# Optimization experiments

Hardware: AMD Instinct MI355X
Metric: run time of the kernel (lower is better)

The kernel has to match this reference:

```python
import jax, jax.numpy as jnp
import numpy as np

VOCAB, D, H, L, SEQ = 32000, 768, 12, 6, 1024
HD = D // H
DFF = 4 * D
EPS = 1e-5


def _ln(x, g, b):
    mu = jnp.mean(x, axis=-1, keepdims=True)
    var = jnp.var(x, axis=-1, keepdims=True)
    return (x - mu) * jax.lax.rsqrt(var + EPS) * g + b


def setup_inputs() -> dict:
    key = jax.random.key(0)
    ks = jax.random.split(key, 10)
    s = lambda *sh: 0.02
    return {
        "idx": jax.random.randint(ks[0], (2, SEQ), 0, VOCAB, dtype=jnp.int64) if jax.config.jax_enable_x64 else jax.random.randint(ks[0], (2, SEQ), 0, VOCAB, dtype=jnp.int32),
        "tok_emb": jax.random.normal(ks[1], (VOCAB, D), jnp.float32) * 0.02,
        "pos_emb": jax.random.normal(ks[2], (SEQ, D), jnp.float32) * 0.02,
        "Wqkv": jax.random.normal(ks[3], (L, D, 3 * D), jnp.float32) * 0.02,
        "bqkv": jnp.zeros((L, 3 * D), jnp.float32),
        "Wo": jax.random.normal(ks[4], (L, D, D), jnp.float32) * 0.02,
        "bo": jnp.zeros((L, D), jnp.float32),
        "ln1_g": jnp.ones((L, D), jnp.float32),
        "ln1_b": jnp.zeros((L, D), jnp.float32),
        "ln2_g": jnp.ones((L, D), jnp.float32),
        "ln2_b": jnp.zeros((L, D), jnp.float32),
        "W1": jax.random.normal(ks[5], (L, D, DFF), jnp.float32) * 0.02,
        "b1": jnp.zeros((L, DFF), jnp.float32),
        "W2": jax.random.normal(ks[6], (L, DFF, D), jnp.float32) * 0.02,
        "b2": jnp.zeros((L, D), jnp.float32),
        "lnf_g": jnp.ones((D,), jnp.float32),
        "lnf_b": jnp.zeros((D,), jnp.float32),
        "Wlm": jax.random.normal(ks[7], (D, VOCAB), jnp.float32) * 0.02,
    }


def _forward(idx, tok_emb, pos_emb, Wqkv, bqkv, Wo, bo, ln1_g, ln1_b,
             ln2_g, ln2_b, W1, b1, W2, b2, lnf_g, lnf_b, Wlm):
    B, T = idx.shape
    x = tok_emb[idx] + pos_emb[None, :T]  # [B,T,D]
    causal = jnp.tril(jnp.ones((T, T), bool))  # [T,T]
    for l in range(L):
        h = _ln(x, ln1_g[l], ln1_b[l])
        qkv = h @ Wqkv[l] + bqkv[l]  # [B,T,3D]
        qkv = qkv.reshape(B, T, 3, H, HD).transpose(2, 0, 3, 1, 4)
        q, k, v = qkv[0], qkv[1], qkv[2]  # each [B,H,T,HD]
        att = jnp.einsum('bhqd,bhkd->bhqk', q, k) / np.sqrt(HD).astype(np.float32)
        att = jnp.where(causal, att, -jnp.inf)
        att = jax.nn.softmax(att, axis=-1)
        o = jnp.einsum('bhqk,bhkd->bhqd', att, v)
        o = o.transpose(0, 2, 1, 3).reshape(B, T, D)
        x = x + o @ Wo[l] + bo[l]
        h = _ln(x, ln2_g[l], ln2_b[l])
        x = x + jax.nn.gelu(h @ W1[l] + b1[l], approximate=False) @ W2[l] + b2[l]
    x = _ln(x, lnf_g, lnf_b)
    return x @ Wlm  # [B,T,VOCAB]


def reference(idx, tok_emb, pos_emb, Wqkv, bqkv, Wo, bo, ln1_g, ln1_b,
              ln2_g, ln2_b, W1, b1, W2, b2, lnf_g, lnf_b, Wlm):
    return _forward(idx, tok_emb, pos_emb, Wqkv, bqkv, Wo, bo, ln1_g, ln1_b,
                    ln2_g, ln2_b, W1, b1, W2, b2, lnf_g, lnf_b, Wlm)
```

## Files before the change

kernel.cpp:

```cpp
#include <hip/hip_runtime.h>
#include <math.h>

#define TT   1024
#define DD   768
#define HH   12
#define LLAY 6
#define DFFN 3072
#define BB   2
#define NTOK (BB*TT)

typedef __bf16 bf16;
typedef __attribute__((ext_vector_type(8))) __bf16 bf16x8;
typedef __attribute__((ext_vector_type(4))) __bf16 bf16x4;
typedef __attribute__((ext_vector_type(4))) float f32x4;

__device__ inline unsigned pack_bf16x2(float a, float b) {
    union { bf16 h[2]; unsigned u; } un;
    un.h[0] = (bf16)a; un.h[1] = (bf16)b;
    return un.u;
}

__device__ inline void gload16(const bf16* g, bf16* l) {
    __builtin_amdgcn_global_load_lds((const void*)g, (void*)l, 16, 0, 0);
}

template<int N> __device__ inline void waitcnt_vm() {
    if constexpr (N == 0) asm volatile("s_waitcnt vmcnt(0)" ::: "memory");
    else if constexpr (N == 3) asm volatile("s_waitcnt vmcnt(3)" ::: "memory");
    else if constexpr (N == 4) asm volatile("s_waitcnt vmcnt(4)" ::: "memory");
}

__global__ __launch_bounds__(256) void embed_kernel(const int* __restrict__ idx,
                                                    const float* __restrict__ tok,
                                                    const float* __restrict__ pos,
                                                    float* __restrict__ x) {
    int bt = blockIdx.x;
    int t  = bt % TT;
    int id = idx[bt];
    const float* te = tok + (size_t)id * DD;
    const float* pe = pos + (size_t)t * DD;
    float* xr = x + (size_t)bt * DD;
    for (int d = threadIdx.x; d < DD; d += 256) xr[d] = te[d] + pe[d];
}

__global__ __launch_bounds__(256) void ln_kernel(const float* __restrict__ in,
                                                 const float* __restrict__ g,
                                                 const float* __restrict__ b,
                                                 bf16* __restrict__ out) {
    const int wid = threadIdx.x >> 6, lane = threadIdx.x & 63;
    const int row = blockIdx.x * 4 + wid;
    const float* xr = in + (size_t)row * DD;
    float4 v[3];
    float s = 0.f, s2 = 0.f;
#pragma unroll
    for (int j = 0; j < 3; ++j) {
        v[j] = *(const float4*)&xr[lane * 4 + 256 * j];
        s  += v[j].x + v[j].y + v[j].z + v[j].w;
        s2 += v[j].x * v[j].x + v[j].y * v[j].y + v[j].z * v[j].z + v[j].w * v[j].w;
    }
    for (int off = 32; off; off >>= 1) { s += __shfl_down(s, off); s2 += __shfl_down(s2, off); }
    s = __shfl(s, 0); s2 = __shfl(s2, 0);
    const float mu = s / (float)DD;
    const float rs = rsqrtf(s2 / (float)DD - mu * mu + 1e-5f);
    bf16* orow = out + (size_t)row * DD;
#pragma unroll
    for (int j = 0; j < 3; ++j) {
        float4 gg = *(const float4*)&g[lane * 4 + 256 * j];
        float4 bb = *(const float4*)&b[lane * 4 + 256 * j];
        bf16x4 o;
        o[0] = (bf16)((v[j].x - mu) * rs * gg.x + bb.x);
        o[1] = (bf16)((v[j].y - mu) * rs * gg.y + bb.y);
        o[2] = (bf16)((v[j].z - mu) * rs * gg.z + bb.z);
        o[3] = (bf16)((v[j].w - mu) * rs * gg.w + bb.w);
        *(bf16x4*)&orow[lane * 4 + 256 * j] = o;
    }
}

__device__ inline void convT_tile64(const float* __restrict__ in, bf16* __restrict__ out,
                                    int K, int N, int k0, int n0) {
    __shared__ float tile[64][65];
    const int c = threadIdx.x & 63, q = threadIdx.x >> 6;
#pragma unroll
    for (int i = 0; i < 16; ++i)
        tile[q + i * 4][c] = in[(size_t)(k0 + q + i * 4) * N + n0 + c];
    __syncthreads();
#pragma unroll
    for (int i = 0; i < 16; ++i)
        out[(size_t)(n0 + q + i * 4) * K + k0 + c] = (bf16)tile[c][q + i * 4];
}

__global__ __launch_bounds__(256) void convT_kernel(const float* __restrict__ in,
                                                    bf16* __restrict__ out,
                                                    int K, int N) {
    convT_tile64(in, out, K, N, blockIdx.y * 64, blockIdx.x * 64);
}

__global__ __launch_bounds__(256) void convT4_kernel(const float* __restrict__ w0,
                                                     const float* __restrict__ w1,
                                                     const float* __restrict__ w2,
                                                     const float* __restrict__ w3,
                                                     bf16* __restrict__ o0,
                                                     bf16* __restrict__ o1,
                                                     bf16* __restrict__ o2,
                                                     bf16* __restrict__ o3) {
    int bid = blockIdx.x;
    const float* in; bf16* out; int K, N, t;
    if (bid < 432)       { in = w0; out = o0; K = 768;  N = 2304; t = bid; }
    else if (bid < 576)  { in = w1; out = o1; K = 768;  N = 768;  t = bid - 432; }
    else if (bid < 1152) { in = w2; out = o2; K = 768;  N = 3072; t = bid - 576; }
    else                 { in = w3; out = o3; K = 3072; N = 768;  t = bid - 1152; }
    int nt = N / 64;
    convT_tile64(in, out, K, N, (t / nt) * 64, (t % nt) * 64);
}

template<int BM, int EPI>
__global__ __launch_bounds__(256) void mgemm(const bf16* __restrict__ A,
                                             const bf16* __restrict__ Bt,
                                             const float* __restrict__ bias,
                                             const float* __restrict__ res,
                                             void* __restrict__ Cout,
                                             bf16* __restrict__ vtout,
                                             int M, int N, int K) {
    constexpr int MF = BM / 32;
    constexpr int NF = 4;
    constexpr int AIT = BM / 64;
    constexpr int STG = AIT + 2;
    constexpr int ASZ = BM * 32;
    constexpr int BUFE = ASZ + 128 * 32;
    __shared__ __align__(16) bf16 smem[3 * BUFE];
    int bm = blockIdx.y * BM;
    int bn = blockIdx.x * 128;
    int tid = threadIdx.x;
    int lane = tid & 63;
    int w = tid >> 6;
    int wr = w >> 1, wc = w & 1;
    int l15 = lane & 15, g = lane >> 4;

    f32x4 acc[MF][NF];
#pragma unroll
    for (int m = 0; m < MF; ++m)
#pragma unroll
        for (int n = 0; n < NF; ++n) acc[m][n] = (f32x4){0.f, 0.f, 0.f, 0.f};

    int r = lane >> 2;
    int koff = ((lane & 3) ^ ((r >> 1) & 3)) * 8;
    const bf16* Ab = A + (size_t)(bm + w * 16 + r) * K + koff;
    const bf16* Bb = Bt + (size_t)(bn + w * 16 + r) * K + koff;

    auto stage = [&](int p, int k0) {
        bf16* base = smem + p * BUFE;
        bf16* Asb = base + w * 16 * 32;
        bf16* Bsb = base + ASZ + w * 16 * 32;
#pragma unroll
        for (int it = 0; it < AIT; ++it)
            gload16(Ab + (size_t)(it * 64) * K + k0, Asb + it * 64 * 32);
#pragma unroll
        for (int it = 0; it < 2; ++it)
            gload16(Bb + (size_t)(it * 64) * K + k0, Bsb + it * 64 * 32);
    };

    stage(0, 0);
    stage(1, 32);
    waitcnt_vm<STG>();
    __builtin_amdgcn_s_barrier();
    int cur = 0;

    for (int k0 = 0; k0 < K; k0 += 32) {
        const bf16* Ac = smem + cur * BUFE;
        const bf16* Bc = Ac + ASZ;
        bf16x8 af[MF], bfv[NF];
#pragma unroll
        for (int m = 0; m < MF; ++m) {
            int row = wr * (BM / 2) + m * 16 + l15;
            int gs = g ^ ((row >> 1) & 3);
            af[m] = *(const bf16x8*)&Ac[row * 32 + gs * 8];
        }
#pragma unroll
        for (int n = 0; n < NF; ++n) {
            int row = wc * 64 + n * 16 + l15;
            int gs = g ^ ((row >> 1) & 3);
            bfv[n] = *(const bf16x8*)&Bc[row * 32 + gs * 8];
        }
        bool st = (k0 + 64 < K);
        if (st) {
            int nxt = cur + 2; if (nxt >= 3) nxt -= 3;
            stage(nxt, k0 + 64);
        }
#pragma unroll
        for (int m = 0; m < MF; ++m)
#pragma unroll
            for (int n = 0; n < NF; ++n)
                acc[m][n] = __builtin_amdgcn_mfma_f32_16x16x32_bf16(af[m], bfv[n], acc[m][n], 0, 0, 0);
        if (st) waitcnt_vm<STG>();
        else    waitcnt_vm<0>();
        __builtin_amdgcn_s_barrier();
        cur = (cur == 2) ? 0 : cur + 1;
    }

    int lq = g * 4;
#pragma unroll
    for (int m = 0; m < MF; ++m) {
#pragma unroll
        for (int n = 0; n < NF; ++n) {
            int col = bn + wc * 64 + n * 16 + l15;
            float bv = bias[col];
            if (EPI == 4 && col >= 2 * DD) {
                int row0 = bm + wr * (BM / 2) + m * 16 + lq;
                int b = row0 >> 10, t0 = row0 & 1023;
                int hd = col - 2 * DD;
                union { bf16 h[4]; unsigned long long u; } pk;
#pragma unroll
                for (int j = 0; j < 4; ++j) pk.h[j] = (bf16)(acc[m][n][j] + bv);
                *(unsigned long long*)&vtout[((size_t)(b * DD + hd)) * TT + t0] = pk.u;
            } else {
#pragma unroll
                for (int j = 0; j < 4; ++j) {
                    int row = bm + wr * (BM / 2) + m * 16 + lq + j;
                    float v = acc[m][n][j] + bv;
                    if (EPI == 2) {
                        ((float*)Cout)[(size_t)row * N + col] = v + res[(size_t)row * N + col];
                    } else if (EPI == 3) {
                        v = 0.5f * v * (1.f + erff(v * 0.70710678118654752f));
                        ((bf16*)Cout)[(size_t)row * N + col] = (bf16)v;
                    } else if (EPI == 1) {
                        ((bf16*)Cout)[(size_t)row * N + col] = (bf16)v;
                    } else {
                        if (col < DD) v *= 0.125f;
                        ((bf16*)Cout)[(size_t)row * N + col] = (bf16)v;
                    }
                }
            }
        }
    }
}

__global__ __launch_bounds__(512, 2) void lmgemm(const bf16* __restrict__ A,
                                                 const bf16* __restrict__ Bt,
                                                 float* __restrict__ C) {
    constexpr int BUFE = 2 * 256 * 64;
    __shared__ __align__(16) bf16 smem[2 * BUFE];
    const int orig = blockIdx.x;
    const int xcd = orig & 7, local = orig >> 3;
    const int bnb = xcd * 16 + (local >> 3);
    if (bnb >= 125) return;
    const int bm = (local & 7) * 256;
    const int bn = bnb * 256;
    const int tid = threadIdx.x;
    const int w = tid >> 6, lane = tid & 63;
    const int wm = w >> 2, wn = w & 3;
    const int l15 = lane & 15, g = lane >> 4;

    const int swzr = (l15 >> 1) & 7;
    const int pc0 = (g ^ swzr) * 8;

    const int r8 = lane >> 3, c8 = lane & 7;
    const bf16* agp[4]; const bf16* bgp[4];
    int aldso[4], bldso[4];
#pragma unroll
    for (int j = 0; j < 4; ++j) {
        int br = w * 32 + j * 8 + r8;
        int swz = (br >> 1) & 7;
        agp[j] = A  + (size_t)(bm + br) * DD + (c8 ^ swz) * 8;
        bgp[j] = Bt + (size_t)(bn + br) * DD + (c8 ^ swz) * 8;
        aldso[j] = (w * 32 + j * 8) * 64;
        bldso[j] = 256 * 64 + (w * 32 + j * 8) * 64;
    }

    f32x4 acc[8][4];
#pragma unroll
    for (int m = 0; m < 8; ++m)
#pragma unroll
        for (int n = 0; n < 4; ++n) acc[m][n] = (f32x4){0.f, 0.f, 0.f, 0.f};

    {
        bf16* base = smem;
#pragma unroll
        for (int j = 0; j < 4; ++j) gload16(agp[j], base + aldso[j]);
#pragma unroll
        for (int j = 0; j < 4; ++j) gload16(bgp[j], base + bldso[j]);
    }
    __syncthreads();
    int cur = 0;

    for (int t = 0; t < 12; ++t) {
        const bf16* Ar = smem + cur * BUFE;
        const bf16* Br = Ar + 256 * 64;
        bf16* nbase = smem + (cur ^ 1) * BUFE;
        const int k0n = (t + 1) * 64;
        const bool st = (t < 11);
        if (st) {
#pragma unroll
            for (int j = 0; j < 4; ++j) gload16(agp[j] + k0n, nbase + aldso[j]);
        }
        bf16x8 af[8], bfv[4];
#pragma unroll
        for (int m = 0; m < 8; ++m)
            af[m] = *(const bf16x8*)&Ar[(wm * 128 + m * 16 + l15) * 64 + pc0];
#pragma unroll
        for (int n = 0; n < 4; ++n)
            bfv[n] = *(const bf16x8*)&Br[(wn * 64 + n * 16 + l15) * 64 + pc0];
        __builtin_amdgcn_s_setprio(1);
#pragma unroll
        for (int m = 0; m < 8; ++m)
#pragma unroll
            for (int n = 0; n < 4; ++n)
                acc[m][n] = __builtin_amdgcn_mfma_f32_16x16x32_bf16(af[m], bfv[n], acc[m][n], 0, 0, 0);
        __builtin_amdgcn_s_setprio(0);
        if (st) {
#pragma unroll
            for (int j = 0; j < 4; ++j) gload16(bgp[j] + k0n, nbase + bldso[j]);
        }
#pragma unroll
        for (int m = 0; m < 8; ++m)
            af[m] = *(const bf16x8*)&Ar[(wm * 128 + m * 16 + l15) * 64 + (pc0 ^ 32)];
#pragma unroll
        for (int n = 0; n < 4; ++n)
            bfv[n] = *(const bf16x8*)&Br[(wn * 64 + n * 16 + l15) * 64 + (pc0 ^ 32)];
        __builtin_amdgcn_s_setprio(1);
#pragma unroll
        for (int m = 0; m < 8; ++m)
#pragma unroll
            for (int n = 0; n < 4; ++n)
                acc[m][n] = __builtin_amdgcn_mfma_f32_16x16x32_bf16(af[m], bfv[n], acc[m][n], 0, 0, 0);
        __builtin_amdgcn_s_setprio(0);
        __syncthreads();
        cur ^= 1;
    }

    float* eb = (float*)smem + w * (16 * 68);
    const int rr = lane >> 2, c0 = (lane & 3) * 16;
#pragma unroll
    for (int mf = 0; mf < 8; ++mf) {
#pragma unroll
        for (int n = 0; n < 4; ++n)
#pragma unroll
            for (int j = 0; j < 4; ++j)
                eb[(g * 4 + j) * 68 + n * 16 + l15] = acc[mf][n][j];
        asm volatile("s_waitcnt lgkmcnt(0)" ::: "memory");
        const float* src = &eb[rr * 68 + c0];
        float* dst = C + (size_t)(bm + wm * 128 + mf * 16 + rr) * 32000 + bn + wn * 64 + c0;
        *(float4*)(dst + 0)  = *(const float4*)(src + 0);
        *(float4*)(dst + 4)  = *(const float4*)(src + 4);
        *(float4*)(dst + 8)  = *(const float4*)(src + 8);
        *(float4*)(dst + 12) = *(const float4*)(src + 12);
    }
}

__global__ __launch_bounds__(256) void fattn_kernel(const bf16* __restrict__ qkv,
                                                    const bf16* __restrict__ vt,
                                                    bf16* __restrict__ o) {
    const int bh = blockIdx.y;
    const int b = bh / HH, h = bh % HH;
    const int qc = gridDim.x - 1 - blockIdx.x;
    const int q0 = qc * 64;
    const int tid = threadIdx.x;
    const int w = tid >> 6, lane = tid & 63;
    const int l15 = lane & 15, g = lane >> 4;

    __shared__ __align__(16) bf16 Ks[64 * 64];
    __shared__ __align__(16) bf16 Vs[64 * 64];
    __shared__ __align__(16) bf16 Ps[4][16 * 64];

    const size_t basebt = (size_t)b * TT;
    const int qw = q0 + w * 16;
    const int qg = qw + l15;

    bf16x8 bq0, bq1;
    {
        const bf16* qp = qkv + (basebt + qw + l15) * 2304 + h * 64 + g * 8;
        bq0 = *(const bf16x8*)(qp);
        bq1 = *(const bf16x8*)(qp + 32);
    }

    float mstate = -1e30f, lstate = 0.f;
    f32x4 oacc[4];
#pragma unroll
    for (int nf = 0; nf < 4; ++nf) oacc[nf] = (f32x4){0.f, 0.f, 0.f, 0.f};

    const int swzA = (l15 & 7) << 4;
    char* const psBase = (char*)&Ps[w][0];

    const int r0 = tid >> 3;
    const int e0 = (tid & 7) * 8;
    bf16x8 kreg[2], vreg[2];
#pragma unroll
    for (int i = 0; i < 2; ++i) {
        int r = r0 + 32 * i;
        kreg[i] = *(const bf16x8*)&qkv[(basebt + r) * 2304 + DD + h * 64 + e0];
        vreg[i] = *(const bf16x8*)&vt[((size_t)bh * 64 + r) * TT + e0];
    }

    const int nchunk = qc + 1;
    for (int c = 0; c < nchunk; ++c) {
        const int kc = c * 64;
#pragma unroll
        for (int i = 0; i < 2; ++i) {
            int r = r0 + 32 * i;
            int swzW = (r & 7) << 4;
            *(bf16x8*)((char*)Ks + r * 128 + ((e0 * 2) ^ swzW)) = kreg[i];
            *(bf16x8*)((char*)Vs + r * 128 + ((e0 * 2) ^ swzW)) = vreg[i];
        }
        __syncthreads();
        if (c + 1 < nchunk) {
            const int kc2 = kc + 64;
#pragma unroll
            for (int i = 0; i < 2; ++i) {
                int r = r0 + 32 * i;
                kreg[i] = *(const bf16x8*)&qkv[(basebt + kc2 + r) * 2304 + DD + h * 64 + e0];
                vreg[i] = *(const bf16x8*)&vt[((size_t)bh * 64 + r) * TT + kc2 + e0];
            }
        }
        if (kc <= qw + 15) {
            f32x4 s[4];
            __builtin_amdgcn_s_setprio(1);
#pragma unroll
            for (int mf = 0; mf < 4; ++mf) {
                char* kr = (char*)Ks + (16 * mf + l15) * 128;
                bf16x8 ka0 = *(const bf16x8*)(kr + ((16 * g) ^ swzA));
                bf16x8 ka1 = *(const bf16x8*)(kr + ((64 + 16 * g) ^ swzA));
                f32x4 a = (f32x4){0.f, 0.f, 0.f, 0.f};
                a = __builtin_amdgcn_mfma_f32_16x16x32_bf16(ka0, bq0, a, 0, 0, 0);
                a = __builtin_amdgcn_mfma_f32_16x16x32_bf16(ka1, bq1, a, 0, 0, 0);
                s[mf] = a;
            }
            __builtin_amdgcn_s_setprio(0);
            if (kc + 63 > qw) {
#pragma unroll
                for (int mf = 0; mf < 4; ++mf)
#pragma unroll
                    for (int j = 0; j < 4; ++j)
                        if (kc + 16 * mf + 4 * g + j > qg) s[mf][j] = -1e30f;
            }
            float cm = -1e30f;
#pragma unroll
            for (int mf = 0; mf < 4; ++mf)
#pragma unroll
                for (int j = 0; j < 4; ++j) cm = fmaxf(cm, s[mf][j]);
            cm = fmaxf(cm, __shfl_xor(cm, 16));
            cm = fmaxf(cm, __shfl_xor(cm, 32));
            float mnew = fmaxf(mstate, cm);
            float sc = __expf(mstate - mnew);
            mstate = mnew;
            float p[4][4];
            float psum = 0.f;
#pragma unroll
            for (int mf = 0; mf < 4; ++mf)
#pragma unroll
                for (int j = 0; j < 4; ++j) { float pv = __expf(s[mf][j] - mnew); p[mf][j] = pv; psum += pv; }
            psum += __shfl_xor(psum, 16);
            psum += __shfl_xor(psum, 32);
            lstate = lstate * sc + psum;
#pragma unroll
            for (int mf = 0; mf < 4; ++mf) {
                unsigned lo = pack_bf16x2(p[mf][0], p[mf][1]);
                unsigned hi = pack_bf16x2(p[mf][2], p[mf][3]);
                char* dst = psBase + l15 * 128 + ((32 * mf + 8 * g) ^ swzA);
                *(unsigned*)dst = lo;
                *(unsigned*)(dst + 4) = hi;
            }
            float s0 = __shfl(sc, 4 * g + 0), s1 = __shfl(sc, 4 * g + 1);
            float s2 = __shfl(sc, 4 * g + 2), s3 = __shfl(sc, 4 * g + 3);
#pragma unroll
            for (int nf = 0; nf < 4; ++nf) {
                oacc[nf][0] *= s0; oacc[nf][1] *= s1; oacc[nf][2] *= s2; oacc[nf][3] *= s3;
            }
            bf16x8 pa0 = *(const bf16x8*)(psBase + l15 * 128 + ((16 * g) ^ swzA));
            bf16x8 pa1 = *(const bf16x8*)(psBase + l15 * 128 + ((64 + 16 * g) ^ swzA));
            __builtin_amdgcn_s_setprio(1);
#pragma unroll
            for (int nf = 0; nf < 4; ++nf) {
                char* vr = (char*)Vs + (16 * nf + l15) * 128;
                bf16x8 vb0 = *(const bf16x8*)(vr + ((16 * g) ^ swzA));
                bf16x8 vb1 = *(const bf16x8*)(vr + ((64 + 16 * g) ^ swzA));
                oacc[nf] = __builtin_amdgcn_mfma_f32_16x16x32_bf16(pa0, vb0, oacc[nf], 0, 0, 0);
                oacc[nf] = __builtin_amdgcn_mfma_f32_16x16x32_bf16(pa1, vb1, oacc[nf], 0, 0, 0);
            }
            __builtin_amdgcn_s_setprio(0);
        }
        __syncthreads();
    }
    float linv = 1.f / lstate;
    float l0 = __shfl(linv, 4 * g + 0), l1 = __shfl(linv, 4 * g + 1);
    float l2 = __shfl(linv, 4 * g + 2), l3 = __shfl(linv, 4 * g + 3);
    float lj[4] = {l0, l1, l2, l3};
#pragma unroll
    for (int j = 0; j < 4; ++j) {
        bf16* orow = o + (size_t)(basebt + qw + 4 * g + j) * DD + h * 64 + l15;
#pragma unroll
        for (int nf = 0; nf < 4; ++nf)
            orow[16 * nf] = (bf16)(oacc[nf][j] * lj[j]);
    }
}

extern "C" void kernel_launch(void* const* d_in, const int* in_sizes, int n_in,
                              void* d_out, int out_size, void* d_ws, size_t ws_size,
                              hipStream_t stream) {
    (void)in_sizes; (void)n_in; (void)out_size; (void)ws_size;
    const int*   idx  = (const int*)d_in[0];
    const float* tok  = (const float*)d_in[1];
    const float* pos  = (const float*)d_in[2];
    const float* Wqkv = (const float*)d_in[3];
    const float* bqkv = (const float*)d_in[4];
    const float* Wo   = (const float*)d_in[5];
    const float* bo   = (const float*)d_in[6];
    const float* ln1g = (const float*)d_in[7];
    const float* ln1b = (const float*)d_in[8];
    const float* ln2g = (const float*)d_in[9];
    const float* ln2b = (const float*)d_in[10];
    const float* W1   = (const float*)d_in[11];
    const float* b1   = (const float*)d_in[12];
    const float* W2   = (const float*)d_in[13];
    const float* b2   = (const float*)d_in[14];
    const float* lnfg = (const float*)d_in[15];
    const float* lnfb = (const float*)d_in[16];
    const float* Wlm  = (const float*)d_in[17];
    float* out = (float*)d_out;

    char* ws = (char*)d_ws;
    float* x     = (float*)(ws);
    bf16*  abuf0 = (bf16*)(ws + 6291456);
    bf16*  abuf1 = (bf16*)(ws + 9437184);
    bf16*  qkvb  = (bf16*)(ws + 22020096);
    bf16*  vtb   = (bf16*)(ws + 31457280);
    bf16*  wbuf  = (bf16*)(ws + 34603008);

    bf16* wq = wbuf;
    bf16* wo = wbuf + 1769472;
    bf16* w1 = wbuf + 2359296;
    bf16* w2 = wbuf + 4718592;

    embed_kernel<<<NTOK, 256, 0, stream>>>(idx, tok, pos, x);

    for (int l = 0; l < LLAY; ++l) {
        convT4_kernel<<<1728, 256, 0, stream>>>(
            Wqkv + (size_t)l * DD * 3 * DD, Wo + (size_t)l * DD * DD,
            W1 + (size_t)l * DD * DFFN, W2 + (size_t)l * DFFN * DD,
            wq, wo, w1, w2);
        ln_kernel<<<NTOK / 4, 256, 0, stream>>>(x, ln1g + l * DD, ln1b + l * DD, abuf0);
        mgemm<128, 4><<<dim3(3 * DD / 128, NTOK / 128), 256, 0, stream>>>(
            abuf0, wq, bqkv + (size_t)l * 3 * DD, nullptr, qkvb, vtb, NTOK, 3 * DD, DD);
        fattn_kernel<<<dim3(TT / 64, BB * HH), 256, 0, stream>>>(qkvb, vtb, abuf0);
        mgemm<64, 2><<<dim3(DD / 128, NTOK / 64), 256, 0, stream>>>(
            abuf0, wo, bo + (size_t)l * DD, x, x, nullptr, NTOK, DD, DD);
        ln_kernel<<<NTOK / 4, 256, 0, stream>>>(x, ln2g + l * DD, ln2b + l * DD, abuf0);
        mgemm<128, 3><<<dim3(DFFN / 128, NTOK / 128), 256, 0, stream>>>(
            abuf0, w1, b1 + (size_t)l * DFFN, nullptr, abuf1, nullptr, NTOK, DFFN, DD);
        mgemm<64, 2><<<dim3(DD / 128, NTOK / 64), 256, 0, stream>>>(
            abuf1, w2, b2 + (size_t)l * DD, x, x, nullptr, NTOK, DD, DFFN);
    }
    ln_kernel<<<NTOK / 4, 256, 0, stream>>>(x, lnfg, lnfb, abuf0);
    convT_kernel<<<dim3(32000 / 64, DD / 64), 256, 0, stream>>>(Wlm, wbuf, DD, 32000);
    lmgemm<<<1024, 512, 0, stream>>>(abuf0, wbuf, out);
}
```

Before: 982.5 us.

## Add 256x128 double-buffered bgemm for QKV/FFN1 and shrink lmgemm K-tile

Adds a new bgemm kernel with 512 threads, 256x128 block tiles, a 32-wide K step and two-stage LDS double buffering, and uses it for the QKV and FFN-up projections in place of the 128-tile mgemm. The lm-head GEMM is also switched from a 64-wide K tile split into two half-steps to a simpler 32-wide K tile with 24 iterations, which halves its LDS footprint. The intent is more per-block reuse and fewer, larger blocks for the projection GEMMs, plus a simpler schedule for the lm-head. The trade-offs are more barriers per unit of K and reduced prefetch depth compared with the three-stage mgemm pipeline.

```diff
diff --git a/kernel.cpp b/kernel.cpp
--- a/kernel.cpp
+++ b/kernel.cpp
@@ -204,8 +204,99 @@
         for (int n = 0; n < NF; ++n) {
             int col = bn + wc * 64 + n * 16 + l15;
             float bv = bias[col];
+#pragma unroll
+            for (int j = 0; j < 4; ++j) {
+                int row = bm + wr * (BM / 2) + m * 16 + lq + j;
+                float v = acc[m][n][j] + bv;
+                if (EPI == 2) {
+                    ((float*)Cout)[(size_t)row * N + col] = v + res[(size_t)row * N + col];
+                } else if (EPI == 3) {
+                    v = 0.5f * v * (1.f + erff(v * 0.70710678118654752f));
+                    ((bf16*)Cout)[(size_t)row * N + col] = (bf16)v;
+                } else {
+                    ((bf16*)Cout)[(size_t)row * N + col] = (bf16)v;
+                }
+            }
+        }
+    }
+    (void)vtout;
+}
+
+template<int EPI>
+__global__ __launch_bounds__(512, 2) void bgemm(const bf16* __restrict__ A,
+                                                const bf16* __restrict__ Bt,
+                                                const float* __restrict__ bias,
+                                                void* __restrict__ Cout,
+                                                bf16* __restrict__ vtout,
+                                                int N, int K) {
+    constexpr int ABUF = 256 * 32;
+    constexpr int BUFE = ABUF + 128 * 32;
+    __shared__ __align__(16) bf16 smem[2 * BUFE];
+    const int bm = blockIdx.y * 256;
+    const int bn = blockIdx.x * 128;
+    const int tid = threadIdx.x;
+    const int w = tid >> 6, lane = tid & 63;
+    const int wm = w >> 1, wn = w & 1;
+    const int l15 = lane & 15, g = lane >> 4;
+
+    const int fcol = (g ^ ((l15 >> 1) & 3)) * 8;
+
+    const int rA = lane >> 2;
+    const int csw = ((lane & 3) ^ ((lane >> 3) & 3)) * 8;
+    const bf16* a0 = A  + (size_t)(bm + w * 16 + rA) * K + csw;
+    const bf16* b0 = Bt + (size_t)(bn + w * 16 + rA) * K + csw;
+    const int ld0 = (w * 16) * 32;
+    const int ld1 = (w * 16 + 128) * 32;
+
+    f32x4 acc[4][4];
+#pragma unroll
+    for (int m = 0; m < 4; ++m)
+#pragma unroll
+        for (int n = 0; n < 4; ++n) acc[m][n] = (f32x4){0.f, 0.f, 0.f, 0.f};
+
+    auto stagef = [&](int p, int kelem) {
+        bf16* base = smem + p * BUFE;
+        gload16(a0 + kelem, base + ld0);
+        gload16(a0 + (size_t)128 * K + kelem, base + ld1);
+        gload16(b0 + kelem, base + ABUF + ld0);
+    };
+
+    stagef(0, 0);
+    __syncthreads();
+    int cur = 0;
+
+    const int NT = K / 32;
+    for (int t = 0; t < NT; ++t) {
+        if (t + 1 < NT) stagef(cur ^ 1, (t + 1) * 32);
+        const bf16* Ar = smem + cur * BUFE;
+        const bf16* Br = Ar + ABUF;
+        bf16x8 af[4], bfv[4];
+#pragma unroll
+        for (int m = 0; m < 4; ++m)
+            af[m] = *(const bf16x8*)&Ar[(wm * 64 + m * 16 + l15) * 32 + fcol];
+#pragma unroll
+        for (int n = 0; n < 4; ++n)
+            bfv[n] = *(const bf16x8*)&Br[(wn * 64 + n * 16 + l15) * 32 + fcol];
+        __builtin_amdgcn_s_setprio(1);
+#pragma unroll
+        for (int m = 0; m < 4; ++m)
+#pragma unroll
+            for (int n = 0; n < 4; ++n)
+                acc[m][n] = __builtin_amdgcn_mfma_f32_16x16x32_bf16(af[m], bfv[n], acc[m][n], 0, 0, 0);
+        __builtin_amdgcn_s_setprio(0);
+        __syncthreads();
+        cur ^= 1;
+    }
+
+    const int lq = g * 4;
+#pragma unroll
+    for (int m = 0; m < 4; ++m) {
+#pragma unroll
+        for (int n = 0; n < 4; ++n) {
+            int col = bn + wn * 64 + n * 16 + l15;
+            float bv = bias[col];
             if (EPI == 4 && col >= 2 * DD) {
-                int row0 = bm + wr * (BM / 2) + m * 16 + lq;
+                int row0 = bm + wm * 64 + m * 16 + lq;
                 int b = row0 >> 10, t0 = row0 & 1023;
                 int hd = col - 2 * DD;
                 union { bf16 h[4]; unsigned long long u; } pk;
@@ -215,14 +306,10 @@
             } else {
 #pragma unroll
                 for (int j = 0; j < 4; ++j) {
-                    int row = bm + wr * (BM / 2) + m * 16 + lq + j;
+                    int row = bm + wm * 64 + m * 16 + lq + j;
                     float v = acc[m][n][j] + bv;
-                    if (EPI == 2) {
-                        ((float*)Cout)[(size_t)row * N + col] = v + res[(size_t)row * N + col];
-                    } else if (EPI == 3) {
+                    if (EPI == 3) {
                         v = 0.5f * v * (1.f + erff(v * 0.70710678118654752f));
-                        ((bf16*)Cout)[(size_t)row * N + col] = (bf16)v;
-                    } else if (EPI == 1) {
                         ((bf16*)Cout)[(size_t)row * N + col] = (bf16)v;
                     } else {
                         if (col < DD) v *= 0.125f;
@@ -237,7 +324,8 @@
 __global__ __launch_bounds__(512, 2) void lmgemm(const bf16* __restrict__ A,
                                                  const bf16* __restrict__ Bt,
                                                  float* __restrict__ C) {
-    constexpr int BUFE = 2 * 256 * 64;
+    constexpr int ABUF = 256 * 32;
+    constexpr int BUFE = 2 * ABUF;
     __shared__ __align__(16) bf16 smem[2 * BUFE];
     const int orig = blockIdx.x;
     const int xcd = orig & 7, local = orig >> 3;
@@ -250,21 +338,14 @@
     const int wm = w >> 2, wn = w & 3;
     const int l15 = lane & 15, g = lane >> 4;
 
-    const int swzr = (l15 >> 1) & 7;
-    const int pc0 = (g ^ swzr) * 8;
-
-    const int r8 = lane >> 3, c8 = lane & 7;
-    const bf16* agp[4]; const bf16* bgp[4];
-    int aldso[4], bldso[4];
-#pragma unroll
-    for (int j = 0; j < 4; ++j) {
-        int br = w * 32 + j * 8 + r8;
-        int swz = (br >> 1) & 7;
-        agp[j] = A  + (size_t)(bm + br) * DD + (c8 ^ swz) * 8;
-        bgp[j] = Bt + (size_t)(bn + br) * DD + (c8 ^ swz) * 8;
-        aldso[j] = (w * 32 + j * 8) * 64;
-        bldso[j] = 256 * 64 + (w * 32 + j * 8) * 64;
-    }
+    const int fcol = (g ^ ((l15 >> 1) & 3)) * 8;
+
+    const int rA = lane >> 2;
+    const int csw = ((lane & 3) ^ ((lane >> 3) & 3)) * 8;
+    const bf16* a0 = A  + (size_t)(bm + w * 16 + rA) * DD + csw;
+    const bf16* b0 = Bt + (size_t)(bn + w * 16 + rA) * DD + csw;
+    const int ld0 = (w * 16) * 32;
+    const int ld1 = (w * 16 + 128) * 32;
 
     f32x4 acc[8][4];
 #pragma unroll
@@ -272,50 +353,29 @@
 #pragma unroll
         for (int n = 0; n < 4; ++n) acc[m][n] = (f32x4){0.f, 0.f, 0.f, 0.f};
 
-    {
-        bf16* base = smem;
-#pragma unroll
-        for (int j = 0; j < 4; ++j) gload16(agp[j], base + aldso[j]);
-#pragma unroll
-        for (int j = 0; j < 4; ++j) gload16(bgp[j], base + bldso[j]);
-    }
+    auto stagef = [&](int p, int kelem) {
+        bf16* base = smem + p * BUFE;
+        gload16(a0 + kelem, base + ld0);
+        gload16(a0 + (size_t)128 * DD + kelem, base + ld1);
+        gload16(b0 + kelem, base + ABUF + ld0);
+        gload16(b0 + (size_t)128 * DD + kelem, base + ABUF + ld1);
+    };
+
+    stagef(0, 0);
     __syncthreads();
     int cur = 0;
 
-    for (int t = 0; t < 12; ++t) {
+    for (int t = 0; t < 24; ++t) {
+        if (t < 23) stagef(cur ^ 1, (t + 1) * 32);
         const bf16* Ar = smem + cur * BUFE;
-        const bf16* Br = Ar + 256 * 64;
-        bf16* nbase = smem + (cur ^ 1) * BUFE;
-        const int k0n = (t + 1) * 64;
-        const bool st = (t < 11);
-        if (st) {
-#pragma unroll
-            for (int j = 0; j < 4; ++j) gload16(agp[j] + k0n, nbase + aldso[j]);
-        }
+        const bf16* Br = Ar + ABUF;
         bf16x8 af[8], bfv[4];
 #pragma unroll
         for (int m = 0; m < 8; ++m)
-            af[m] = *(const bf16x8*)&Ar[(wm * 128 + m * 16 + l15) * 64 + pc0];
+            af[m] = *(const bf16x8*)&Ar[(wm * 128 + m * 16 + l15) * 32 + fcol];
 #pragma unroll
         for (int n = 0; n < 4; ++n)
-            bfv[n] = *(const bf16x8*)&Br[(wn * 64 + n * 16 + l15) * 64 + pc0];
-        __builtin_amdgcn_s_setprio(1);
-#pragma unroll
-        for (int m = 0; m < 8; ++m)
-#pragma unroll
-            for (int n = 0; n < 4; ++n)
-                acc[m][n] = __builtin_amdgcn_mfma_f32_16x16x32_bf16(af[m], bfv[n], acc[m][n], 0, 0, 0);
-        __builtin_amdgcn_s_setprio(0);
-        if (st) {
-#pragma unroll
-            for (int j = 0; j < 4; ++j) gload16(bgp[j] + k0n, nbase + bldso[j]);
-        }
-#pragma unroll
-        for (int m = 0; m < 8; ++m)
-            af[m] = *(const bf16x8*)&Ar[(wm * 128 + m * 16 + l15) * 64 + (pc0 ^ 32)];
-#pragma unroll
-        for (int n = 0; n < 4; ++n)
-            bfv[n] = *(const bf16x8*)&Br[(wn * 64 + n * 16 + l15) * 64 + (pc0 ^ 32)];
+            bfv[n] = *(const bf16x8*)&Br[(wn * 64 + n * 16 + l15) * 32 + fcol];
         __builtin_amdgcn_s_setprio(1);
 #pragma unroll
         for (int m = 0; m < 8; ++m)
@@ -537,14 +597,14 @@
             W1 + (size_t)l * DD * DFFN, W2 + (size_t)l * DFFN * DD,
             wq, wo, w1, w2);
         ln_kernel<<<NTOK / 4, 256, 0, stream>>>(x, ln1g + l * DD, ln1b + l * DD, abuf0);
-        mgemm<128, 4><<<dim3(3 * DD / 128, NTOK / 128), 256, 0, stream>>>(
-            abuf0, wq, bqkv + (size_t)l * 3 * DD, nullptr, qkvb, vtb, NTOK, 3 * DD, DD);
+        bgemm<4><<<dim3(3 * DD / 128, NTOK / 256), 512, 0, stream>>>(
+            abuf0, wq, bqkv + (size_t)l * 3 * DD, qkvb, vtb, 3 * DD, DD);
         fattn_kernel<<<dim3(TT / 64, BB * HH), 256, 0, stream>>>(qkvb, vtb, abuf0);
         mgemm<64, 2><<<dim3(DD / 128, NTOK / 64), 256, 0, stream>>>(
             abuf0, wo, bo + (size_t)l * DD, x, x, nullptr, NTOK, DD, DD);
         ln_kernel<<<NTOK / 4, 256, 0, stream>>>(x, ln2g + l * DD, ln2b + l * DD, abuf0);
-        mgemm<128, 3><<<dim3(DFFN / 128, NTOK / 128), 256, 0, stream>>>(
-            abuf0, w1, b1 + (size_t)l * DFFN, nullptr, abuf1, nullptr, NTOK, DFFN, DD);
+        bgemm<3><<<dim3(DFFN / 128, NTOK / 256), 512, 0, stream>>>(
+            abuf0, w1, b1 + (size_t)l * DFFN, abuf1, nullptr, DFFN, DD);
         mgemm<64, 2><<<dim3(DD / 128, NTOK / 64), 256, 0, stream>>>(
             abuf1, w2, b2 + (size_t)l * DD, x, x, nullptr, NTOK, DD, DFFN);
     }
```

Measured after the change: 1.012 ms. +3.0%, slower.
